# Kernel tuning notes

Hardware: AMD Instinct MI355X
Metric: run time of the kernel (lower is better)

## Reference

```python
import jax, jax.numpy as jnp
import numpy as np

IN_CH = 384
HEAD_DIM = 32
MAX_SEQ = 64          # P, tokens per window
N_HEADS = IN_CH // HEAD_DIM
PART = int(np.sqrt(MAX_SEQ))  # 8, window side
SCALE = HEAD_DIM ** -0.5


def _relative_position_index():
    # Swin relative position index, [P*P] int
    h = np.arange(PART)
    coords = np.stack(np.meshgrid(h, h, indexing='ij')).reshape(2, -1)  # [2, P]
    rel = coords[:, :, None] - coords[:, None, :]                        # [2, P, P]
    rel = rel.transpose(1, 2, 0).astype(np.int64)
    rel[:, :, 0] += PART - 1
    rel[:, :, 1] += PART - 1
    rel[:, :, 0] *= 2 * PART - 1
    return rel.sum(-1).reshape(-1)  # [P*P]

REL_IDX = jnp.asarray(_relative_position_index())


def setup_inputs() -> dict:
    key = jax.random.key(0)
    ks = jax.random.split(key, 6)
    B, G, P, D = 32, 64, MAX_SEQ, IN_CH
    x = jax.random.normal(ks[0], (B, G, P, D), dtype=jnp.float32)
    Wqkv = jax.random.normal(ks[1], (D, 3 * D), dtype=jnp.float32) * (D ** -0.5)
    bqkv = jnp.zeros((3 * D,), dtype=jnp.float32)
    Wm = jax.random.normal(ks[2], (D, D), dtype=jnp.float32) * (D ** -0.5)
    bm = jnp.zeros((D,), dtype=jnp.float32)
    # torch init is zeros; use small normal so bias actually affects the output
    rel_table = jax.random.normal(ks[3], ((2 * PART - 1) ** 2, N_HEADS), dtype=jnp.float32) * 0.02
    return {"x": x, "Wqkv": Wqkv, "bqkv": bqkv, "Wm": Wm, "bm": bm, "rel_table": rel_table}


def reference(x, Wqkv, bqkv, Wm, bm, rel_table):
    B, G, P, D = x.shape
    H, DH = N_HEADS, HEAD_DIM
    qkv = x @ Wqkv + bqkv                                   # [B,G,P,3D]
    q, k, v = jnp.split(qkv, 3, axis=-1)
    q = q.reshape(B, G, P, H, DH) * SCALE
    k = k.reshape(B, G, P, H, DH)
    v = v.reshape(B, G, P, H, DH)
    attn = jnp.einsum('bgihd,bgjhd->bghij', q, k)           # [B,G,H,P,P]
    bias = rel_table[REL_IDX].reshape(P, P, H).transpose(2, 0, 1)  # [H,P,P]
    attn = jax.nn.softmax(attn + bias[None, None], axis=-1)
    out = jnp.einsum('bghij,bgjhd->bgihd', attn, v)         # [B,G,P,H,DH]
    out = out.reshape(B, G, P, D)
    return out @ Wm + bm
```

## Files before the change

### kernel.cpp

```cpp
#include <hip/hip_runtime.h>
#include <stdint.h>


typedef __attribute__((ext_vector_type(4))) float f32x4;
typedef __attribute__((ext_vector_type(4))) short s16x4;
typedef __attribute__((ext_vector_type(8))) short s16x8;

#define DEVI static __device__ __forceinline__

DEVI unsigned short f2bf(float f) {
  union { float f; uint32_t u; } v; v.f = f;
  return (unsigned short)((v.u + 0x7FFFu + ((v.u >> 16) & 1u)) >> 16);
}

DEVI f32x4 zero4() { f32x4 z; z[0] = 0.f; z[1] = 0.f; z[2] = 0.f; z[3] = 0.f; return z; }

#if defined(__has_builtin)
#if __has_builtin(__builtin_amdgcn_mfma_f32_16x16x16bf16_1k)
#define MFMA16_BUILTIN 1
#endif
#if __has_builtin(__builtin_amdgcn_global_load_lds)
#define HAS_GLLDS 1
#endif
#endif

DEVI f32x4 mfma16(s16x4 a, s16x4 b, f32x4 c) {
#ifdef MFMA16_BUILTIN
  return __builtin_amdgcn_mfma_f32_16x16x16bf16_1k(a, b, c, 0, 0, 0);
#else
  asm volatile("v_mfma_f32_16x16x16_bf16 %0, %1, %2, %0" : "+v"(c) : "v"(a), "v"(b));
  return c;
#endif
}

DEVI f32x4 mfma32(s16x8 a, s16x8 b, f32x4 c) {
  return __builtin_amdgcn_mfma_f32_16x16x32_bf16(a, b, c, 0, 0, 0);
}

DEVI void stage1k(const unsigned short* g_lane, unsigned short* lds_base) {
#ifdef HAS_GLLDS
  __builtin_amdgcn_global_load_lds(
      (const __attribute__((address_space(1))) unsigned int*)g_lane,
      (__attribute__((address_space(3))) unsigned int*)lds_base, 16, 0, 0);
#else
  *(s16x8*)(lds_base + (threadIdx.x & 63) * 8) = *(const s16x8*)g_lane;
#endif
}

__global__ void prep_wqkvT(const float* __restrict__ W, unsigned short* __restrict__ WT) {
  int t = blockIdx.x * 256 + threadIdx.x;
  if (t >= 1152 * 384) return;
  int n = t / 384, k = t - n * 384;
  float s = (n < 384) ? 0.17677669529663687f : 1.0f;
  WT[t] = f2bf(W[(size_t)k * 1152 + n] * s);
}

__global__ void prep_wmT(const float* __restrict__ W, unsigned short* __restrict__ WT) {
  int t = blockIdx.x * 256 + threadIdx.x;
  if (t >= 384 * 384) return;
  int n = t / 384, k = t - n * 384;
  WT[t] = f2bf(W[(size_t)k * 384 + n]);
}

__global__ void prep_bqkv(const float* __restrict__ b, float* __restrict__ bs) {
  int t = blockIdx.x * 256 + threadIdx.x;
  if (t >= 1152) return;
  bs[t] = b[t] * ((t < 384) ? 0.17677669529663687f : 1.0f);
}

__global__ void prep_biasF(const float* __restrict__ rel, float* __restrict__ biasF) {
  int t = blockIdx.x * 256 + threadIdx.x;
  if (t >= 12288) return;
  int h = t >> 10;
  int r = (t >> 6) & 15;
  int lane = t & 63;
  int jt = r >> 2, it = r & 3;
  int lg = lane >> 4, lr = lane & 15;
  int i = it * 16 + lr;
#pragma unroll
  for (int e = 0; e < 4; ++e) {
    int j = jt * 16 + lg * 4 + e;
    int idx = ((i >> 3) - (j >> 3) + 7) * 15 + ((i & 7) - (j & 7) + 7);
    biasF[t * 4 + e] = rel[idx * 12 + h];
  }
}

__global__ void fill_val(float* o, int n, float v) {
  int t = blockIdx.x * 256 + threadIdx.x;
  if (t < n) o[t] = v;
}

__global__ __launch_bounds__(256) void conv_bf16(const float* __restrict__ x,
                                                 unsigned short* __restrict__ xb) {
  const size_t nchunk = 131072UL * 384 / 8;
  const size_t stride = (size_t)gridDim.x * blockDim.x;
  for (size_t i = (size_t)blockIdx.x * blockDim.x + threadIdx.x; i < nchunk; i += stride) {
    f32x4 a = *(const f32x4*)(x + i * 8);
    f32x4 b = *(const f32x4*)(x + i * 8 + 4);
    s16x8 p;
    p[0] = (short)f2bf(a[0]); p[1] = (short)f2bf(a[1]);
    p[2] = (short)f2bf(a[2]); p[3] = (short)f2bf(a[3]);
    p[4] = (short)f2bf(b[0]); p[5] = (short)f2bf(b[1]);
    p[6] = (short)f2bf(b[2]); p[7] = (short)f2bf(b[3]);
    *(s16x8*)(xb + i * 8) = p;
  }
}

template <bool QKV_EPI>
__global__ __launch_bounds__(256) void gemm_k(const unsigned short* __restrict__ A,
                                              const unsigned short* __restrict__ BT,
                                              const float* __restrict__ bias,
                                              void* __restrict__ Cv) {
  constexpr int K = 384;
  constexpr int NT = QKV_EPI ? 9 : 3;
  constexpr int N = NT * 128;
  __shared__ unsigned short As[128 * 64];
  __shared__ unsigned short Bs[128 * 64];
  const int bid = blockIdx.x;
  const int swz = (bid & 7) * (NT * 128) + (bid >> 3);
  const int n0 = (swz % NT) * 128;
  const int m0 = (swz / NT) * 128;
  const int tid = threadIdx.x;
  const int lane = tid & 63, wv = tid >> 6;
  const int wr = wv >> 1, wc = wv & 1;
  const int lg = lane >> 4, lr = lane & 15;

  const unsigned short* Ag = A + (size_t)(m0 + wv * 32 + (lane >> 3)) * K + (lane & 7) * 8;
  const unsigned short* Bg = BT + (size_t)(n0 + wv * 32 + (lane >> 3)) * K + (lane & 7) * 8;

  f32x4 acc[4][4];
#pragma unroll
  for (int i = 0; i < 4; ++i)
#pragma unroll
    for (int j = 0; j < 4; ++j) acc[i][j] = zero4();

  for (int k0 = 0; k0 < K; k0 += 64) {
#pragma unroll
    for (int c = 0; c < 4; ++c)
      stage1k(Ag + (size_t)(c * 8) * K + k0, &As[(wv * 32 + c * 8) * 64]);
#pragma unroll
    for (int c = 0; c < 4; ++c)
      stage1k(Bg + (size_t)(c * 8) * K + k0, &Bs[(wv * 32 + c * 8) * 64]);
    __syncthreads();
#pragma unroll
    for (int kk = 0; kk < 64; kk += 32) {
      s16x8 af[4], bf[4];
#pragma unroll
      for (int mt = 0; mt < 4; ++mt)
        af[mt] = *(const s16x8*)&As[(wr * 64 + 16 * mt + lr) * 64 + kk + 8 * lg];
#pragma unroll
      for (int nt = 0; nt < 4; ++nt)
        bf[nt] = *(const s16x8*)&Bs[(wc * 64 + 16 * nt + lr) * 64 + kk + 8 * lg];
#pragma unroll
      for (int mt = 0; mt < 4; ++mt)
#pragma unroll
        for (int nt = 0; nt < 4; ++nt)
          acc[mt][nt] = mfma32(af[mt], bf[nt], acc[mt][nt]);
    }
    __syncthreads();
  }

  const int crow = m0 + wr * 64 + 4 * lg;
  const int ccol = n0 + wc * 64 + lr;
  if constexpr (QKV_EPI) {
    const int sel = n0 / 384;
    const int window = crow >> 6;
    const int t0 = crow & 63;
    unsigned short* qkv = (unsigned short*)Cv;
#pragma unroll
    for (int nt = 0; nt < 4; ++nt) {
      const int col = ccol + 16 * nt;
      const int hcol = col - sel * 384;
      const int h = hcol >> 5, d = hcol & 31;
      const float bv = bias[col];
      unsigned short* base = qkv + (((size_t)window * 12 + h) * 3 + sel) * 2048;
#pragma unroll
      for (int mt = 0; mt < 4; ++mt) {
        if (sel < 2) {
#pragma unroll
          for (int e = 0; e < 4; ++e)
            base[(t0 + 16 * mt + e) * 32 + d] = f2bf(acc[mt][nt][e] + bv);
        } else {
          s16x4 pk;
#pragma unroll
          for (int e = 0; e < 4; ++e) pk[e] = (short)f2bf(acc[mt][nt][e] + bv);
          *(s16x4*)&base[d * 64 + t0 + 16 * mt] = pk;
        }
      }
    }
  } else {
    float* C = (float*)Cv;
#pragma unroll
    for (int mt = 0; mt < 4; ++mt)
#pragma unroll
      for (int nt = 0; nt < 4; ++nt) {
        const int col = ccol + 16 * nt;
        const float bv = bias[col];
#pragma unroll
        for (int e = 0; e < 4; ++e)
          C[(size_t)(crow + 16 * mt + e) * N + col] = acc[mt][nt][e] + bv;
      }
  }
}

__global__ __launch_bounds__(256) void attn_k(const unsigned short* __restrict__ qkv,
                                              const float* __restrict__ biasF,
                                              unsigned short* __restrict__ attnout) {
  const int lane = threadIdx.x & 63;
  const int wv = threadIdx.x >> 6;
  const int wh = blockIdx.x * 4 + wv;
  const int window = wh / 12;
  const int h = wh - window * 12;
  const int lg = lane >> 4, lr = lane & 15;

  const unsigned short* hb = qkv + (size_t)wh * 6144;
  const unsigned short* Qh = hb;
  const unsigned short* Kh = hb + 2048;
  const unsigned short* Vth = hb + 4096;

  s16x8 ka[4], qb[4];
#pragma unroll
  for (int jt = 0; jt < 4; ++jt)
    ka[jt] = *(const s16x8*)&Kh[(jt * 16 + lr) * 32 + 8 * lg];
#pragma unroll
  for (int it = 0; it < 4; ++it)
    qb[it] = *(const s16x8*)&Qh[(it * 16 + lr) * 32 + 8 * lg];

  f32x4 c[4][4];
#pragma unroll
  for (int a = 0; a < 4; ++a)
#pragma unroll
    for (int b2 = 0; b2 < 4; ++b2) c[a][b2] = zero4();

#pragma unroll
  for (int jt = 0; jt < 4; ++jt)
#pragma unroll
    for (int it = 0; it < 4; ++it)
      c[jt][it] = mfma32(ka[jt], qb[it], c[jt][it]);

  const f32x4* bF = (const f32x4*)biasF + ((size_t)h * 16) * 64 + lane;
#pragma unroll
  for (int jt = 0; jt < 4; ++jt)
#pragma unroll
    for (int it = 0; it < 4; ++it)
      c[jt][it] += bF[(jt * 4 + it) * 64];

  s16x4 pb[4][4];
#pragma unroll
  for (int it = 0; it < 4; ++it) {
    float m = -3.0e38f;
#pragma unroll
    for (int jt = 0; jt < 4; ++jt)
#pragma unroll
      for (int e = 0; e < 4; ++e) m = fmaxf(m, c[jt][it][e]);
    m = fmaxf(m, __shfl_xor(m, 16));
    m = fmaxf(m, __shfl_xor(m, 32));
    float s = 0.f;
#pragma unroll
    for (int jt = 0; jt < 4; ++jt)
#pragma unroll
      for (int e = 0; e < 4; ++e) {
        float p = __expf(c[jt][it][e] - m);
        c[jt][it][e] = p;
        s += p;
      }
    s += __shfl_xor(s, 16);
    s += __shfl_xor(s, 32);
    const float inv = 1.f / s;
#pragma unroll
    for (int jt = 0; jt < 4; ++jt) {
      s16x4 pk;
#pragma unroll
      for (int e = 0; e < 4; ++e) pk[e] = (short)f2bf(c[jt][it][e] * inv);
      pb[jt][it] = pk;
    }
  }

  f32x4 o[2][4];
#pragma unroll
  for (int a = 0; a < 2; ++a)
#pragma unroll
    for (int b2 = 0; b2 < 4; ++b2) o[a][b2] = zero4();

#pragma unroll
  for (int jt = 0; jt < 4; ++jt) {
    s16x4 va[2];
#pragma unroll
    for (int dt = 0; dt < 2; ++dt)
      va[dt] = *(const s16x4*)&Vth[(dt * 16 + lr) * 64 + jt * 16 + 4 * lg];
#pragma unroll
    for (int dt = 0; dt < 2; ++dt)
#pragma unroll
      for (int it = 0; it < 4; ++it)
        o[dt][it] = mfma16(va[dt], pb[jt][it], o[dt][it]);
  }

  unsigned short* ob = attnout + (size_t)window * 64 * 384;
#pragma unroll
  for (int dt = 0; dt < 2; ++dt)
#pragma unroll
    for (int it = 0; it < 4; ++it) {
      s16x4 pk;
#pragma unroll
      for (int e = 0; e < 4; ++e) pk[e] = (short)f2bf(o[dt][it][e]);
      *(s16x4*)&ob[(size_t)(it * 16 + lr) * 384 + h * 32 + dt * 16 + 4 * lg] = pk;
    }
}

extern "C" void kernel_launch(void* const* d_in, const int* in_sizes, int n_in,
                              void* d_out, int out_size, void* d_ws, size_t ws_size,
                              hipStream_t stream) {
  const float* x = (const float*)d_in[0];
  const float* Wqkv = (const float*)d_in[1];
  const float* bqkv = (const float*)d_in[2];
  const float* Wm = (const float*)d_in[3];
  const float* bm = (const float*)d_in[4];
  const float* rel = (const float*)d_in[5];

  const size_t M = 131072;
  char* ws = (char*)d_ws;
  size_t off = 0;
  unsigned short* qkv = (unsigned short*)(ws + off);   off += M * 1152 * 2;
  unsigned short* xb = (unsigned short*)(ws + off);    off += M * 384 * 2;
  unsigned short* WqkvT = (unsigned short*)(ws + off); off += 1152 * 384 * 2;
  unsigned short* WmT = (unsigned short*)(ws + off);   off += 384 * 384 * 2;
  float* biasF = (float*)(ws + off);                   off += 12 * 16 * 64 * 4 * 4;
  float* bqkvs = (float*)(ws + off);                   off += 1152 * 4;
  unsigned short* attnout = xb;

  if (ws_size < off) {
    fill_val<<<(out_size + 255) / 256, 256, 0, stream>>>((float*)d_out, out_size, 12345.0f);
    return;
  }

  prep_wqkvT<<<(1152 * 384 + 255) / 256, 256, 0, stream>>>(Wqkv, WqkvT);
  prep_wmT<<<(384 * 384 + 255) / 256, 256, 0, stream>>>(Wm, WmT);
  prep_bqkv<<<5, 256, 0, stream>>>(bqkv, bqkvs);
  prep_biasF<<<48, 256, 0, stream>>>(rel, biasF);
  conv_bf16<<<2048, 256, 0, stream>>>(x, xb);

  gemm_k<true><<<9216, 256, 0, stream>>>(xb, WqkvT, bqkvs, qkv);
  attn_k<<<6144, 256, 0, stream>>>(qkv, biasF, attnout);
  gemm_k<false><<<3072, 256, 0, stream>>>(attnout, WmT, bm, d_out);
}
```

Baseline: 522.9 us.

## Double-buffer GEMM K-loop and stage Q/K epilogue through swizzled LDS

The GEMM main loop now keeps two LDS buffers, issuing global-to-LDS loads for the next K slice before computing on the current one. Partial vmcnt waits and raw barriers let the loads overlap with the MFMA work. The Q/K epilogue also writes its bf16 tile into XOR-swizzled LDS first, then emits 16-byte coalesced stores per head, replacing scattered 2-byte stores. The cost is doubled LDS use, which may lower occupancy, plus hand-written waitcnt logic that depends on the exact number of outstanding loads.

```diff
diff --git a/kernel.cpp b/kernel.cpp
--- a/kernel.cpp
+++ b/kernel.cpp
@@ -114,8 +114,7 @@
   constexpr int K = 384;
   constexpr int NT = QKV_EPI ? 9 : 3;
   constexpr int N = NT * 128;
-  __shared__ unsigned short As[128 * 64];
-  __shared__ unsigned short Bs[128 * 64];
+  __shared__ unsigned short sm[2][16384];
   const int bid = blockIdx.x;
   const int swz = (bid & 7) * (NT * 128) + (bid >> 3);
   const int n0 = (swz % NT) * 128;
@@ -134,53 +133,98 @@
 #pragma unroll
     for (int j = 0; j < 4; ++j) acc[i][j] = zero4();
 
-  for (int k0 = 0; k0 < K; k0 += 64) {
-#pragma unroll
-    for (int c = 0; c < 4; ++c)
-      stage1k(Ag + (size_t)(c * 8) * K + k0, &As[(wv * 32 + c * 8) * 64]);
-#pragma unroll
-    for (int c = 0; c < 4; ++c)
-      stage1k(Bg + (size_t)(c * 8) * K + k0, &Bs[(wv * 32 + c * 8) * 64]);
-    __syncthreads();
+  auto STAGE = [&](int buf, int k0) {
+#pragma unroll
+    for (int c2 = 0; c2 < 4; ++c2)
+      stage1k(Ag + (size_t)(c2 * 8) * K + k0, &sm[buf][(wv * 32 + c2 * 8) * 64]);
+#pragma unroll
+    for (int c2 = 0; c2 < 4; ++c2)
+      stage1k(Bg + (size_t)(c2 * 8) * K + k0, &sm[buf][8192 + (wv * 32 + c2 * 8) * 64]);
+  };
+  auto COMPUTE = [&](int buf) {
 #pragma unroll
     for (int kk = 0; kk < 64; kk += 32) {
       s16x8 af[4], bf[4];
 #pragma unroll
       for (int mt = 0; mt < 4; ++mt)
-        af[mt] = *(const s16x8*)&As[(wr * 64 + 16 * mt + lr) * 64 + kk + 8 * lg];
+        af[mt] = *(const s16x8*)&sm[buf][(wr * 64 + 16 * mt + lr) * 64 + kk + 8 * lg];
 #pragma unroll
       for (int nt = 0; nt < 4; ++nt)
-        bf[nt] = *(const s16x8*)&Bs[(wc * 64 + 16 * nt + lr) * 64 + kk + 8 * lg];
+        bf[nt] = *(const s16x8*)&sm[buf][8192 + (wc * 64 + 16 * nt + lr) * 64 + kk + 8 * lg];
 #pragma unroll
       for (int mt = 0; mt < 4; ++mt)
 #pragma unroll
         for (int nt = 0; nt < 4; ++nt)
           acc[mt][nt] = mfma32(af[mt], bf[nt], acc[mt][nt]);
     }
-    __syncthreads();
-  }
+  };
+
+  STAGE(0, 0);
+  int cur = 0;
+#pragma unroll 1
+  for (int t = 0; t < 5; ++t) {
+    STAGE(cur ^ 1, (t + 1) * 64);
+    asm volatile("s_waitcnt vmcnt(8)" ::: "memory");
+    __builtin_amdgcn_s_barrier();
+    asm volatile("" ::: "memory");
+    COMPUTE(cur);
+    asm volatile("" ::: "memory");
+    __builtin_amdgcn_s_barrier();
+    cur ^= 1;
+  }
+  asm volatile("s_waitcnt vmcnt(0)" ::: "memory");
+  __builtin_amdgcn_s_barrier();
+  asm volatile("" ::: "memory");
+  COMPUTE(cur);
 
   const int crow = m0 + wr * 64 + 4 * lg;
   const int ccol = n0 + wc * 64 + lr;
   if constexpr (QKV_EPI) {
     const int sel = n0 / 384;
-    const int window = crow >> 6;
-    const int t0 = crow & 63;
     unsigned short* qkv = (unsigned short*)Cv;
-#pragma unroll
-    for (int nt = 0; nt < 4; ++nt) {
-      const int col = ccol + 16 * nt;
-      const int hcol = col - sel * 384;
-      const int h = hcol >> 5, d = hcol & 31;
-      const float bv = bias[col];
-      unsigned short* base = qkv + (((size_t)window * 12 + h) * 3 + sel) * 2048;
-#pragma unroll
-      for (int mt = 0; mt < 4; ++mt) {
-        if (sel < 2) {
-#pragma unroll
-          for (int e = 0; e < 4; ++e)
-            base[(t0 + 16 * mt + e) * 32 + d] = f2bf(acc[mt][nt][e] + bv);
-        } else {
+    if (sel < 2) {
+      unsigned short* tile = &sm[0][0];
+#pragma unroll
+      for (int nt = 0; nt < 4; ++nt) {
+        const int cc = wc * 64 + 16 * nt + lr;
+        const float bv = bias[n0 + cc];
+#pragma unroll
+        for (int mt = 0; mt < 4; ++mt) {
+#pragma unroll
+          for (int e = 0; e < 4; ++e) {
+            const int r = wr * 64 + 16 * mt + 4 * lg + e;
+            tile[r * 128 + (cc ^ ((r & 7) << 3))] = f2bf(acc[mt][nt][e] + bv);
+          }
+        }
+      }
+      __syncthreads();
+      const int hbase = (n0 - sel * 384) >> 5;
+#pragma unroll
+      for (int rr = 0; rr < 2; ++rr) {
+        const int tr = wv * 32 + rr * 16 + (lane >> 2);
+        const int gtok = m0 + tr;
+        const int w2 = gtok >> 6, t0r = gtok & 63;
+#pragma unroll
+        for (int hh = 0; hh < 4; ++hh) {
+          const int chunk = hh * 4 + (lane & 3);
+          s16x8 v = *(const s16x8*)&tile[tr * 128 + ((chunk * 8) ^ ((tr & 7) << 3))];
+          unsigned short* dst = qkv + (((size_t)w2 * 12 + hbase + hh) * 3 + sel) * 2048 +
+                                t0r * 32 + (lane & 3) * 8;
+          *(s16x8*)dst = v;
+        }
+      }
+    } else {
+      const int window = crow >> 6;
+      const int t0 = crow & 63;
+#pragma unroll
+      for (int nt = 0; nt < 4; ++nt) {
+        const int col = ccol + 16 * nt;
+        const int hcol = col - 768;
+        const int h = hcol >> 5, d = hcol & 31;
+        const float bv = bias[col];
+        unsigned short* base = qkv + (((size_t)window * 12 + h) * 3 + 2) * 2048;
+#pragma unroll
+        for (int mt = 0; mt < 4; ++mt) {
           s16x4 pk;
 #pragma unroll
           for (int e = 0; e < 4; ++e) pk[e] = (short)f2bf(acc[mt][nt][e] + bv);
```

After: 485.6 us. 1.08x faster.
